# Kernel tuning notes

Measured on AMD Instinct MI355X. Metric: run time of the kernel, lower is better.

Reference implementation:

```python
import jax, jax.numpy as jnp
import numpy as np

B, S, IN, H, NH = 64, 512, 512, 1024, 4
HD = H // NH
A, HID = 18, 1024
EPS = 1e-5


def _ln(x, w, eps=EPS):
    mu = jnp.mean(x, axis=-1, keepdims=True)
    var = jnp.mean((x - mu) ** 2, axis=-1, keepdims=True)
    return (x - mu) * jax.lax.rsqrt(var + eps) * w


def setup_inputs() -> dict:
    key = jax.random.key(0)
    ks = jax.random.split(key, 12)
    g = lambda k, shape, s: jax.random.normal(k, shape, jnp.float32) * s
    return {
        "obs": g(ks[0], (B, S, IN), 1.0),
        "slstm_state": jnp.zeros((4, B, H), jnp.float32),  # (y, c, n, m)
        "W_in": g(ks[1], (H, IN), IN ** -0.5),
        "b_in": jnp.zeros((H,), jnp.float32),
        "ln1_w": jnp.ones((H,), jnp.float32),
        "w_gates": g(ks[2], (4, NH, HD, HD), HD ** -0.5),  # i,f,z,o headwise input proj
        "R": g(ks[3], (NH, HD, 4, HD), HD ** -0.5),        # headwise recurrent kernel
        "b_gates": jnp.zeros((4, H), jnp.float32),
        "gn_w": jnp.ones((H,), jnp.float32),               # multi-head group norm weight
        "ln_post_w": jnp.ones((H,), jnp.float32),          # post-blocks norm
        "W_hid": g(ks[4], (HID, H), H ** -0.5), "b_hid": jnp.zeros((HID,), jnp.float32),
        "W_pol": g(ks[5], (HID, HID), HID ** -0.5), "b_pol": jnp.zeros((HID,), jnp.float32),
        "W_val": g(ks[6], (HID, HID), HID ** -0.5), "b_val": jnp.zeros((HID,), jnp.float32),
        "W_act": g(ks[7], (A, HID), 0.01), "b_act": jnp.zeros((A,), jnp.float32),
        "W_v": g(ks[8], (1, HID), HID ** -0.5), "b_v": jnp.zeros((1,), jnp.float32),
    }


def reference(obs, slstm_state, W_in, b_in, ln1_w, w_gates, R, b_gates, gn_w,
              ln_post_w, W_hid, b_hid, W_pol, b_pol, W_val, b_val, W_act, b_act, W_v, b_v):
    b, s, _ = obs.shape
    # input projection (input_size != hidden_size -> nn.Linear)
    x_proj = obs @ W_in.T + b_in                      # (B,S,H)
    # sLSTM block pre-norm
    xn = _ln(x_proj, ln1_w)
    xh = xn.reshape(b, s, NH, HD)
    # headwise (block-diagonal) gate input preactivations, time-major for scan
    gx = jnp.einsum('bsnd,gnde->sgbne', xh, w_gates)  # (S,4,B,NH,HD)
    bg = b_gates.reshape(4, 1, NH, HD)
    st = slstm_state.reshape(4, b, NH, HD)

    def step(carry, gx_t):
        h, c, n, m = carry
        raw = gx_t + jnp.einsum('bnd,ndge->gbne', h, R) + bg  # (4,B,NH,HD)
        iraw, fraw, zraw, oraw = raw
        logfplusm = m + jax.nn.log_sigmoid(fraw)
        mnew = jnp.maximum(iraw, logfplusm)
        i = jnp.exp(iraw - mnew)
        f = jnp.exp(logfplusm - mnew)
        cnew = f * c + i * jnp.tanh(zraw)
        nnew = f * n + i
        hnew = jax.nn.sigmoid(oraw) * cnew / nnew
        return (hnew, cnew, nnew, mnew), hnew

    _, ys = jax.lax.scan(step, (st[0], st[1], st[2], st[3]), gx)  # (S,B,NH,HD)
    y = jnp.transpose(ys, (1, 0, 2, 3))               # (B,S,NH,HD)
    # multi-head group norm over head_dim, then residual
    mu = jnp.mean(y, axis=-1, keepdims=True)
    var = jnp.mean((y - mu) ** 2, axis=-1, keepdims=True)
    y_gn = (y - mu) * jax.lax.rsqrt(var + EPS) * gn_w.reshape(NH, HD)
    out = x_proj + y_gn.reshape(b, s, H)
    out = _ln(out, ln_post_w)                         # post_blocks_norm
    # actor-critic heads
    hh = jax.nn.relu(out @ W_hid.T + b_hid)
    hp = jax.nn.relu(hh @ W_pol.T + b_pol)
    hv = jax.nn.relu(hh @ W_val.T + b_val)
    logits = hp @ W_act.T + b_act                     # (B,S,A)
    value = hv @ W_v.T + b_v                          # (B,S,1)
    return logits, value
```

## Files before the change

kernel.cpp:

```cpp
#include <hip/hip_runtime.h>
#include <cstdint>
#include <cstddef>

#define B_ 64
#define S_ 512
#define IN_ 512
#define H_ 1024
#define NH_ 4
#define HD_ 256
#define A_ 18
#define HID_ 1024
#define TCH_ 128
#define NCH_ (S_ / TCH_)

using short8 = __attribute__((ext_vector_type(8))) short;
using f32x4  = __attribute__((ext_vector_type(4))) float;

__device__ __forceinline__ unsigned short f2bf(float f) {
  union { float f; unsigned u; } c; c.f = f;
  unsigned r = c.u + 0x7FFFu + ((c.u >> 16) & 1u);
  return (unsigned short)(r >> 16);
}
__device__ __forceinline__ float bf2f(unsigned short h) {
  union { unsigned u; float f; } c; c.u = ((unsigned)h) << 16;
  return c.f;
}
__device__ __forceinline__ unsigned pk2(float a, float b) {
  return (unsigned)f2bf(a) | ((unsigned)f2bf(b) << 16);
}
__device__ __forceinline__ float dot2(unsigned a, unsigned b, float c) {
  float d;
  asm("v_dot2_f32_bf16 %0, %1, %2, %3" : "=v"(d) : "v"(a), "v"(b), "v"(c));
  return d;
}

__global__ __launch_bounds__(256) void rtrans_k(const float* __restrict__ R,
                                                unsigned* __restrict__ Rbb,
                                                unsigned* __restrict__ Rl) {
  const int i = blockIdx.x * 256 + threadIdx.x;
  const int dp = i & 127;
  const int e = (i >> 7) & 255;
  const int g = (i >> 15) & 3;
  const int nh = i >> 17;
  const float* rp = R + (((size_t)nh * 256 + 2 * dp) * 4 + g) * 256 + e;
  unsigned lo = f2bf(rp[0]), hi = f2bf(rp[1024]);
  unsigned v = lo | (hi << 16);
  Rbb[i] = v;
  if (dp >= 96) {
    int j = (dp - 96) >> 1, p = (dp - 96) & 1;
    int col = g * 256 + e;
    Rl[((size_t)(j * 4 + nh) * 1024 + col) * 2 + p] = v;
  }
}

__global__ __launch_bounds__(256) void wgt_k(const float* __restrict__ wg,
                                             unsigned short* __restrict__ wgb) {
  const int i = blockIdx.x * 256 + threadIdx.x;
  const int k = i & 255;
  const int e = (i >> 8) & 255;
  const int g = (i >> 16) & 3;
  const int nh = i >> 18;
  wgb[i] = f2bf(wg[(((size_t)(g * 4 + nh) * 256 + k) * 256) + e]);
}

__global__ __launch_bounds__(256) void wbf_k(const float* __restrict__ src,
                                             unsigned short* __restrict__ dst, int n) {
  int i = blockIdx.x * 256 + threadIdx.x;
  if (i < n) dst[i] = f2bf(src[i]);
}

__global__ __launch_bounds__(256) void rowstats_k(const unsigned short* __restrict__ x,
                                                  float* __restrict__ rs) {
  const int r = blockIdx.x, tid = threadIdx.x;
  const int lane = tid & 63, wave = tid >> 6;
  ushort4 u = *(const ushort4*)(x + (size_t)r * H_ + tid * 4);
  float v0 = bf2f(u.x), v1 = bf2f(u.y), v2 = bf2f(u.z), v3 = bf2f(u.w);
  float s1 = v0 + v1 + v2 + v3;
  float s2 = v0 * v0 + v1 * v1 + v2 * v2 + v3 * v3;
#pragma unroll
  for (int off = 32; off; off >>= 1) { s1 += __shfl_xor(s1, off); s2 += __shfl_xor(s2, off); }
  __shared__ float a1[4], a2[4];
  if (lane == 0) { a1[wave] = s1; a2[wave] = s2; }
  __syncthreads();
  if (tid == 0) {
    float S1 = a1[0] + a1[1] + a1[2] + a1[3];
    float S2 = a2[0] + a2[1] + a2[2] + a2[3];
    float mu = S1 * (1.f / H_);
    float var = S2 * (1.f / H_) - mu * mu;
    rs[r * 2] = mu;
    rs[r * 2 + 1] = rsqrtf(var + 1e-5f);
  }
}

template <int AMODE, int BMODE, bool RELU, int OUTMODE>
__global__ __launch_bounds__(256) void mgemm_k(
    const void* __restrict__ Av, const void* __restrict__ Wv,
    const float* __restrict__ bias, const float* __restrict__ rs,
    const float* __restrict__ lnw, unsigned short* __restrict__ Cb,
    int K, int lda, int chunk) {
  __shared__ uint4 As4[4][128];
  __shared__ uint4 Bs4[4][128];
  const int tid = threadIdx.x;
  const int lane = tid & 63, wave = tid >> 6;
  const int wr = wave >> 1, wc = wave & 1;
  const int col0 = blockIdx.y * 128;
  int nh = 0, g = 0, aoff = 0, bb = 0;
  size_t wbase = 0;
  if constexpr (OUTMODE == 1) {
    int z = blockIdx.z; nh = z >> 2; g = z & 3;
    aoff = nh * HD_;
    bb = blockIdx.x;
    wbase = (size_t)(nh * 4 + g) * 256 * 256;
  }
  auto arow = [&](int mm) -> int {
    if constexpr (OUTMODE == 1) return bb * 512 + chunk * TCH_ + mm;
    else return (int)blockIdx.x * 128 + mm;
  };
  f32x4 acc[4][4];
#pragma unroll
  for (int m = 0; m < 4; ++m)
#pragma unroll
    for (int n = 0; n < 4; ++n) acc[m][n] = 0.f;

  const int sm = tid >> 1;
  const int sh = tid & 1;

  for (int k0 = 0; k0 < K; k0 += 32) {
    {
      int rg = arow(sm);
      unsigned pk[8];
      if constexpr (AMODE == 0) {
        const float* ap = (const float*)Av + (size_t)rg * lda + k0 + sh * 16;
#pragma unroll
        for (int q = 0; q < 4; ++q) {
          float4 f = ((const float4*)ap)[q];
          pk[2 * q] = pk2(f.x, f.y); pk[2 * q + 1] = pk2(f.z, f.w);
        }
      } else if constexpr (AMODE == 1) {
        const uint4* ap = (const uint4*)((const unsigned short*)Av + (size_t)rg * lda + aoff + k0 + sh * 16);
        uint4 u0 = ap[0], u1 = ap[1];
        pk[0] = u0.x; pk[1] = u0.y; pk[2] = u0.z; pk[3] = u0.w;
        pk[4] = u1.x; pk[5] = u1.y; pk[6] = u1.z; pk[7] = u1.w;
      } else {
        const uint4* ap = (const uint4*)((const unsigned short*)Av + (size_t)rg * lda + aoff + k0 + sh * 16);
        uint4 u0 = ap[0], u1 = ap[1];
        unsigned w8[8] = {u0.x, u0.y, u0.z, u0.w, u1.x, u1.y, u1.z, u1.w};
        float mu = rs[rg * 2], rstd = rs[rg * 2 + 1];
        const float* lw = lnw + aoff + k0 + sh * 16;
#pragma unroll
        for (int q = 0; q < 8; ++q) {
          float lo = (bf2f((unsigned short)w8[q]) - mu) * rstd * lw[2 * q];
          float hi = (bf2f((unsigned short)(w8[q] >> 16)) - mu) * rstd * lw[2 * q + 1];
          pk[q] = pk2(lo, hi);
        }
      }
      As4[2 * sh][sm]     = uint4{pk[0], pk[1], pk[2], pk[3]};
      As4[2 * sh + 1][sm] = uint4{pk[4], pk[5], pk[6], pk[7]};
    }
    {
      unsigned pk[8];
      if constexpr (BMODE == 0) {
        const float* wp = (const float*)Wv + (size_t)(col0 + sm) * K + k0 + sh * 16;
#pragma unroll
        for (int q = 0; q < 4; ++q) {
          float4 f = ((const float4*)wp)[q];
          pk[2 * q] = pk2(f.x, f.y); pk[2 * q + 1] = pk2(f.z, f.w);
        }
      } else if constexpr (BMODE == 1) {
        const uint4* wp = (const uint4*)((const unsigned short*)Wv + wbase + (size_t)(col0 + sm) * 256 + k0 + sh * 16);
        uint4 u0 = wp[0], u1 = wp[1];
        pk[0] = u0.x; pk[1] = u0.y; pk[2] = u0.z; pk[3] = u0.w;
        pk[4] = u1.x; pk[5] = u1.y; pk[6] = u1.z; pk[7] = u1.w;
      } else {
        const uint4* wp = (const uint4*)((const unsigned short*)Wv + (size_t)(col0 + sm) * K + k0 + sh * 16);
        uint4 u0 = wp[0], u1 = wp[1];
        pk[0] = u0.x; pk[1] = u0.y; pk[2] = u0.z; pk[3] = u0.w;
        pk[4] = u1.x; pk[5] = u1.y; pk[6] = u1.z; pk[7] = u1.w;
      }
      Bs4[2 * sh][sm]     = uint4{pk[0], pk[1], pk[2], pk[3]};
      Bs4[2 * sh + 1][sm] = uint4{pk[4], pk[5], pk[6], pk[7]};
    }
    __syncthreads();
    short8 af[4], bfv[4];
#pragma unroll
    for (int m = 0; m < 4; ++m)
      af[m] = *(const short8*)&As4[lane >> 4][wr * 64 + m * 16 + (lane & 15)];
#pragma unroll
    for (int n = 0; n < 4; ++n)
      bfv[n] = *(const short8*)&Bs4[lane >> 4][wc * 64 + n * 16 + (lane & 15)];
#pragma unroll
    for (int m = 0; m < 4; ++m)
#pragma unroll
      for (int n = 0; n < 4; ++n)
        acc[m][n] = __builtin_amdgcn_mfma_f32_16x16x32_bf16(af[m], bfv[n], acc[m][n], 0, 0, 0);
    __syncthreads();
  }
  if constexpr (OUTMODE == 0) {
#pragma unroll
    for (int n = 0; n < 4; ++n) {
      int c = col0 + wc * 64 + n * 16 + (lane & 15);
      float bc = bias ? bias[c] : 0.f;
#pragma unroll
      for (int m = 0; m < 4; ++m) {
        int r0 = arow(wr * 64 + m * 16 + ((lane >> 4) << 2));
#pragma unroll
        for (int i = 0; i < 4; ++i) {
          float v = acc[m][n][i] + bc;
          if constexpr (RELU) v = fmaxf(v, 0.f);
          Cb[(size_t)(r0 + i) * 1024 + c] = f2bf(v);
        }
      }
    }
  } else {
#pragma unroll
    for (int n = 0; n < 4; ++n) {
      int e = col0 + wc * 64 + n * 16 + (lane & 15);
#pragma unroll
      for (int m = 0; m < 4; ++m) {
        int sl0 = wr * 64 + m * 16 + ((lane >> 4) << 2);
#pragma unroll
        for (int i = 0; i < 4; ++i) {
          int sl = sl0 + i;
          size_t base = (size_t)(sl * 64 + bb) * 4096 + nh * 1024 + g * 256;
          Cb[base + e] = f2bf(acc[m][n][i]);
        }
      }
    }
  }
}

__global__ __launch_bounds__(1024, 1) void scan_k(
    const unsigned short* __restrict__ gxc, const unsigned* __restrict__ Rbb,
    const unsigned* __restrict__ Rl, const float* __restrict__ bgates,
    float* __restrict__ state, unsigned short* __restrict__ y, int chunk) {
  const int tid = threadIdx.x;
  const int bid = blockIdx.x;
  const int nh = bid >> 6, b = bid & 63;
  const int g = tid >> 8;
  __shared__ uint2 Rlds[16][1024];
  __shared__ float rawf[1024];
  __shared__ alignas(16) unsigned short hsu[256];

#pragma unroll
  for (int j = 0; j < 16; ++j) {
    const uint2* src = (const uint2*)Rl + (size_t)(j * 4 + nh) * 1024 + tid;
    Rlds[j][tid] = *src;
  }
  unsigned rcol[96];
  {
    const unsigned* rp = Rbb + ((size_t)nh * 1024 + tid) * 128;
#pragma unroll
    for (int i = 0; i < 96; ++i) rcol[i] = rp[i];
  }
  const float bg = bgates[g * H_ + nh * HD_ + (tid & 255)];

  const size_t sbase = (size_t)b * H_ + nh * HD_ + tid;
  float c_ = 0.f, n_ = 0.f, m_ = 0.f, hlast = 0.f;
  if (tid < 256) {
    hlast = state[sbase];
    c_ = state[65536 + sbase];
    n_ = state[2 * 65536 + sbase];
    m_ = state[3 * 65536 + sbase];
    hsu[tid] = f2bf(hlast);
  }
  __syncthreads();

  const unsigned short* gp = gxc + ((size_t)b * 4 + nh) * 1024 + tid;
  unsigned short* yp = y + ((size_t)(chunk * TCH_) * 64 + b) * H_ + nh * HD_;

  unsigned short gcur = gp[0];

  for (int t = 0; t < TCH_; ++t) {
    float acc = bf2f(gcur) + bg;
    if (t < TCH_ - 1) gcur = gp[(size_t)(t + 1) * 262144];
    const uint4* h4 = (const uint4*)hsu;
#pragma unroll
    for (int q = 0; q < 24; ++q) {
      uint4 hu = h4[q];
      acc = dot2(rcol[4 * q + 0], hu.x, acc);
      acc = dot2(rcol[4 * q + 1], hu.y, acc);
      acc = dot2(rcol[4 * q + 2], hu.z, acc);
      acc = dot2(rcol[4 * q + 3], hu.w, acc);
    }
#pragma unroll
    for (int s = 0; s < 8; ++s) {
      uint4 hu = h4[24 + s];
      uint2 r0 = Rlds[2 * s][tid];
      uint2 r1 = Rlds[2 * s + 1][tid];
      acc = dot2(r0.x, hu.x, acc);
      acc = dot2(r0.y, hu.y, acc);
      acc = dot2(r1.x, hu.z, acc);
      acc = dot2(r1.y, hu.w, acc);
    }
    float val;
    if (g == 0) {
      val = acc;
    } else if (g == 1) {
      float ls = -log1pf(expf(-fabsf(acc)));
      if (acc < 0.f) ls += acc;
      val = ls;
    } else if (g == 2) {
      val = tanhf(acc);
    } else {
      val = 1.f / (1.f + expf(-acc));
    }
    rawf[tid] = val;
    __syncthreads();
    if (tid < 256) {
      float iraw = rawf[tid];
      float ls   = rawf[256 + tid];
      float tz   = rawf[512 + tid];
      float sg   = rawf[768 + tid];
      float lfm = m_ + ls;
      float mnew = fmaxf(iraw, lfm);
      float iv = expf(iraw - mnew);
      float fv = expf(lfm - mnew);
      c_ = fv * c_ + iv * tz;
      n_ = fv * n_ + iv;
      m_ = mnew;
      hlast = sg * c_ / n_;
      unsigned short hb = f2bf(hlast);
      hsu[tid] = hb;
      yp[(size_t)t * 65536 + tid] = hb;
    }
    __syncthreads();
  }
  if (tid < 256) {
    state[sbase] = hlast;
    state[65536 + sbase] = c_;
    state[2 * 65536 + sbase] = n_;
    state[3 * 65536 + sbase] = m_;
  }
}

__global__ __launch_bounds__(256) void post_k(
    const unsigned short* __restrict__ y, const unsigned short* __restrict__ xp,
    const float* __restrict__ gnw, const float* __restrict__ lpw,
    unsigned short* __restrict__ outb) {
  const int r = blockIdx.x;
  const int b = r >> 9, s = r & 511;
  const int tid = threadIdx.x;
  const int lane = tid & 63, wave = tid >> 6;
  ushort4 yu = *(const ushort4*)(y + (size_t)(s * 64 + b) * H_ + tid * 4);
  float v[4] = {bf2f(yu.x), bf2f(yu.y), bf2f(yu.z), bf2f(yu.w)};
  float s1 = v[0] + v[1] + v[2] + v[3];
  float s2 = v[0] * v[0] + v[1] * v[1] + v[2] * v[2] + v[3] * v[3];
#pragma unroll
  for (int off = 32; off; off >>= 1) { s1 += __shfl_xor(s1, off); s2 += __shfl_xor(s2, off); }
  float mu = s1 * (1.f / HD_);
  float rstd = rsqrtf(s2 * (1.f / HD_) - mu * mu + 1e-5f);
  float4 g4 = *(const float4*)(gnw + tid * 4);
  ushort4 xu = *(const ushort4*)(xp + (size_t)r * H_ + tid * 4);
  float o[4];
  o[0] = fmaf((v[0] - mu) * rstd, g4.x, bf2f(xu.x));
  o[1] = fmaf((v[1] - mu) * rstd, g4.y, bf2f(xu.y));
  o[2] = fmaf((v[2] - mu) * rstd, g4.z, bf2f(xu.z));
  o[3] = fmaf((v[3] - mu) * rstd, g4.w, bf2f(xu.w));
  float t1 = o[0] + o[1] + o[2] + o[3];
  float t2 = o[0] * o[0] + o[1] * o[1] + o[2] * o[2] + o[3] * o[3];
#pragma unroll
  for (int off = 32; off; off >>= 1) { t1 += __shfl_xor(t1, off); t2 += __shfl_xor(t2, off); }
  __shared__ float a1[4], a2[4];
  if (lane == 0) { a1[wave] = t1; a2[wave] = t2; }
  __syncthreads();
  float T1 = a1[0] + a1[1] + a1[2] + a1[3];
  float T2 = a2[0] + a2[1] + a2[2] + a2[3];
  float MU = T1 * (1.f / H_);
  float RS = rsqrtf(T2 * (1.f / H_) - MU * MU + 1e-5f);
  float4 w4 = *(const float4*)(lpw + tid * 4);
  ushort4 res = {f2bf((o[0] - MU) * RS * w4.x), f2bf((o[1] - MU) * RS * w4.y),
                 f2bf((o[2] - MU) * RS * w4.z), f2bf((o[3] - MU) * RS * w4.w)};
  *(ushort4*)(outb + (size_t)r * H_ + tid * 4) = res;
}

__global__ __launch_bounds__(256) void heads_k(
    const unsigned short* __restrict__ hp, const unsigned short* __restrict__ hv,
    const float* __restrict__ Wact, const float* __restrict__ bact,
    const float* __restrict__ Wv, const float* __restrict__ bv,
    float* __restrict__ dout) {
  const int lane = threadIdx.x & 63, wave = threadIdx.x >> 6;
  const int r = blockIdx.x * 4 + wave;
  const unsigned short* hpr = hp + (size_t)r * HID_;
  const unsigned short* hvr = hv + (size_t)r * HID_;
  float acc[A_];
#pragma unroll
  for (int j = 0; j < A_; ++j) acc[j] = 0.f;
  float accv = 0.f;
  for (int i = 0; i < 16; ++i) {
    int k = i * 64 + lane;
    float hpv = bf2f(hpr[k]);
    float hvv = bf2f(hvr[k]);
#pragma unroll
    for (int j = 0; j < A_; ++j) acc[j] = fmaf(hpv, Wact[j * HID_ + k], acc[j]);
    accv = fmaf(hvv, Wv[k], accv);
  }
#pragma unroll
  for (int j = 0; j < A_; ++j)
#pragma unroll
    for (int off = 32; off; off >>= 1) acc[j] += __shfl_xor(acc[j], off);
#pragma unroll
  for (int off = 32; off; off >>= 1) accv += __shfl_xor(accv, off);
  if (lane == 0) {
#pragma unroll
    for (int j = 0; j < A_; ++j) dout[(size_t)r * A_ + j] = acc[j] + bact[j];
    dout[589824 + r] = accv + bv[0];
  }
}

extern "C" void kernel_launch(void* const* d_in, const int* in_sizes, int n_in,
                              void* d_out, int out_size, void* d_ws, size_t ws_size,
                              hipStream_t stream) {
  const float* obs   = (const float*)d_in[0];
  const float* st    = (const float*)d_in[1];
  const float* W_in  = (const float*)d_in[2];
  const float* b_in  = (const float*)d_in[3];
  const float* ln1w  = (const float*)d_in[4];
  const float* wg    = (const float*)d_in[5];
  const float* R     = (const float*)d_in[6];
  const float* bgat  = (const float*)d_in[7];
  const float* gnw   = (const float*)d_in[8];
  const float* lpw   = (const float*)d_in[9];
  const float* W_hid = (const float*)d_in[10];
  const float* b_hid = (const float*)d_in[11];
  const float* W_pol = (const float*)d_in[12];
  const float* b_pol = (const float*)d_in[13];
  const float* W_val = (const float*)d_in[14];
  const float* b_val = (const float*)d_in[15];
  const float* W_act = (const float*)d_in[16];
  const float* b_act = (const float*)d_in[17];
  const float* W_v   = (const float*)d_in[18];
  const float* b_v   = (const float*)d_in[19];

  const size_t NEEDED = 214958080;
  if (ws_size < NEEDED) return;
  char* ws = (char*)d_ws;
  unsigned short* xproj = (unsigned short*)(ws + 0);
  unsigned short* gxc   = (unsigned short*)(ws + 67108864);
  unsigned short* ybuf  = (unsigned short*)(ws + 134217728);
  float* statebuf       = (float*)(ws + 201326592);
  float* rstat          = (float*)(ws + 202375168);
  unsigned* Rbb         = (unsigned*)(ws + 202899456);
  unsigned short* wgb   = (unsigned short*)(ws + 204996608);
  unsigned* Rl          = (unsigned*)(ws + 207093760);
  unsigned short* wib   = (unsigned short*)(ws + 207618048);
  unsigned short* whb   = (unsigned short*)(ws + 208666624);
  unsigned short* wpb   = (unsigned short*)(ws + 210763776);
  unsigned short* wvb   = (unsigned short*)(ws + 212860928);
  unsigned short* outb  = gxc;
  unsigned short* hh    = xproj;
  unsigned short* hp    = ybuf;
  unsigned short* hv    = gxc;
  float* dout = (float*)d_out;

  hipMemcpyAsync(statebuf, st, 4 * 65536 * sizeof(float), hipMemcpyDeviceToDevice, stream);
  rtrans_k<<<2048, 256, 0, stream>>>(R, Rbb, Rl);
  wgt_k<<<4096, 256, 0, stream>>>(wg, wgb);
  wbf_k<<<2048, 256, 0, stream>>>(W_in, wib, 524288);
  wbf_k<<<4096, 256, 0, stream>>>(W_hid, whb, 1048576);
  wbf_k<<<4096, 256, 0, stream>>>(W_pol, wpb, 1048576);
  wbf_k<<<4096, 256, 0, stream>>>(W_val, wvb, 1048576);
  mgemm_k<0, 2, false, 0><<<dim3(256, 8), 256, 0, stream>>>(
      obs, wib, b_in, nullptr, nullptr, xproj, 512, 512, 0);
  rowstats_k<<<32768, 256, 0, stream>>>(xproj, rstat);
  for (int c = 0; c < NCH_; ++c) {
    mgemm_k<2, 1, false, 1><<<dim3(64, 2, 16), 256, 0, stream>>>(
        xproj, wgb, nullptr, rstat, ln1w, gxc, 256, 1024, c);
    scan_k<<<256, 1024, 0, stream>>>(gxc, Rbb, Rl, bgat, statebuf, ybuf, c);
  }
  post_k<<<32768, 256, 0, stream>>>(ybuf, xproj, gnw, lpw, outb);
  mgemm_k<1, 2, true, 0><<<dim3(256, 8), 256, 0, stream>>>(
      outb, whb, b_hid, nullptr, nullptr, hh, 1024, 1024, 0);
  mgemm_k<1, 2, true, 0><<<dim3(256, 8), 256, 0, stream>>>(
      hh, wpb, b_pol, nullptr, nullptr, hp, 1024, 1024, 0);
  mgemm_k<1, 2, true, 0><<<dim3(256, 8), 256, 0, stream>>>(
      hh, wvb, b_val, nullptr, nullptr, hv, 1024, 1024, 0);
  heads_k<<<8192, 256, 0, stream>>>(hp, hv, W_act, b_act, W_v, b_v, dout);
}
```

Before: 2.178 ms.

## Halve scan block size so each thread computes two gate columns

The recurrent scan kernel now runs with 512 threads per block instead of 1024, and each thread owns two of the 1024 gate columns. Each thread holds two register-resident slices of R, shares each h-vector LDS load across both dot products, and runs two independent accumulation chains. Because of the column split, the per-gate activation branches collapse to two fixed cases per thread. The goal is more instruction-level parallelism and fewer waves per block barrier. The cost is roughly double the register pressure (192 R registers plus accumulators), which risks spills, and launch bounds of 512,2 may not be achievable given the LDS footprint.

```diff
diff --git a/kernel.cpp b/kernel.cpp
--- a/kernel.cpp
+++ b/kernel.cpp
@@ -229,30 +229,36 @@
   }
 }
 
-__global__ __launch_bounds__(1024, 1) void scan_k(
+__global__ __launch_bounds__(512, 2) void scan_k(
     const unsigned short* __restrict__ gxc, const unsigned* __restrict__ Rbb,
     const unsigned* __restrict__ Rl, const float* __restrict__ bgates,
     float* __restrict__ state, unsigned short* __restrict__ y, int chunk) {
   const int tid = threadIdx.x;
   const int bid = blockIdx.x;
   const int nh = bid >> 6, b = bid & 63;
-  const int g = tid >> 8;
+  const int col0 = tid, col1 = tid + 512;
+  const int g0 = col0 >> 8, g1 = col1 >> 8;
   __shared__ uint2 Rlds[16][1024];
   __shared__ float rawf[1024];
   __shared__ alignas(16) unsigned short hsu[256];
 
 #pragma unroll
-  for (int j = 0; j < 16; ++j) {
-    const uint2* src = (const uint2*)Rl + (size_t)(j * 4 + nh) * 1024 + tid;
-    Rlds[j][tid] = *src;
-  }
-  unsigned rcol[96];
+  for (int it = 0; it < 32; ++it) {
+    int idx = it * 512 + tid;
+    int j = idx >> 10, col = idx & 1023;
+    Rlds[j][col] = ((const uint2*)Rl)[(size_t)(j * 4 + nh) * 1024 + col];
+  }
+  unsigned rc0[96], rc1[96];
   {
-    const unsigned* rp = Rbb + ((size_t)nh * 1024 + tid) * 128;
-#pragma unroll
-    for (int i = 0; i < 96; ++i) rcol[i] = rp[i];
-  }
-  const float bg = bgates[g * H_ + nh * HD_ + (tid & 255)];
+    const unsigned* rp0 = Rbb + ((size_t)nh * 1024 + col0) * 128;
+    const unsigned* rp1 = Rbb + ((size_t)nh * 1024 + col1) * 128;
+#pragma unroll
+    for (int i = 0; i < 96; ++i) rc0[i] = rp0[i];
+#pragma unroll
+    for (int i = 0; i < 96; ++i) rc1[i] = rp1[i];
+  }
+  const float bg0 = bgates[g0 * H_ + nh * HD_ + (col0 & 255)];
+  const float bg1 = bgates[g1 * H_ + nh * HD_ + (col1 & 255)];
 
   const size_t sbase = (size_t)b * H_ + nh * HD_ + tid;
   float c_ = 0.f, n_ = 0.f, m_ = 0.f, hlast = 0.f;
@@ -265,46 +271,63 @@
   }
   __syncthreads();
 
-  const unsigned short* gp = gxc + ((size_t)b * 4 + nh) * 1024 + tid;
+  const unsigned short* gp0 = gxc + ((size_t)b * 4 + nh) * 1024 + col0;
+  const unsigned short* gp1 = gp0 + 512;
   unsigned short* yp = y + ((size_t)(chunk * TCH_) * 64 + b) * H_ + nh * HD_;
 
-  unsigned short gcur = gp[0];
+  unsigned short gc0 = gp0[0], gc1 = gp1[0];
 
   for (int t = 0; t < TCH_; ++t) {
-    float acc = bf2f(gcur) + bg;
-    if (t < TCH_ - 1) gcur = gp[(size_t)(t + 1) * 262144];
+    float acc0 = bf2f(gc0) + bg0;
+    float acc1 = bf2f(gc1) + bg1;
+    if (t < TCH_ - 1) {
+      gc0 = gp0[(size_t)(t + 1) * 262144];
+      gc1 = gp1[(size_t)(t + 1) * 262144];
+    }
     const uint4* h4 = (const uint4*)hsu;
 #pragma unroll
     for (int q = 0; q < 24; ++q) {
       uint4 hu = h4[q];
-      acc = dot2(rcol[4 * q + 0], hu.x, acc);
-      acc = dot2(rcol[4 * q + 1], hu.y, acc);
-      acc = dot2(rcol[4 * q + 2], hu.z, acc);
-      acc = dot2(rcol[4 * q + 3], hu.w, acc);
+      acc0 = dot2(rc0[4 * q + 0], hu.x, acc0);
+      acc1 = dot2(rc1[4 * q + 0], hu.x, acc1);
+      acc0 = dot2(rc0[4 * q + 1], hu.y, acc0);
+      acc1 = dot2(rc1[4 * q + 1], hu.y, acc1);
+      acc0 = dot2(rc0[4 * q + 2], hu.z, acc0);
+      acc1 = dot2(rc1[4 * q + 2], hu.z, acc1);
+      acc0 = dot2(rc0[4 * q + 3], hu.w, acc0);
+      acc1 = dot2(rc1[4 * q + 3], hu.w, acc1);
     }
 #pragma unroll
     for (int s = 0; s < 8; ++s) {
       uint4 hu = h4[24 + s];
-      uint2 r0 = Rlds[2 * s][tid];
-      uint2 r1 = Rlds[2 * s + 1][tid];
-      acc = dot2(r0.x, hu.x, acc);
-      acc = dot2(r0.y, hu.y, acc);
-      acc = dot2(r1.x, hu.z, acc);
-      acc = dot2(r1.y, hu.w, acc);
-    }
-    float val;
-    if (g == 0) {
-      val = acc;
-    } else if (g == 1) {
-      float ls = -log1pf(expf(-fabsf(acc)));
-      if (acc < 0.f) ls += acc;
-      val = ls;
-    } else if (g == 2) {
-      val = tanhf(acc);
+      uint2 a0 = Rlds[2 * s][col0];
+      uint2 a1 = Rlds[2 * s + 1][col0];
+      uint2 b0 = Rlds[2 * s][col1];
+      uint2 b1 = Rlds[2 * s + 1][col1];
+      acc0 = dot2(a0.x, hu.x, acc0);
+      acc1 = dot2(b0.x, hu.x, acc1);
+      acc0 = dot2(a0.y, hu.y, acc0);
+      acc1 = dot2(b0.y, hu.y, acc1);
+      acc0 = dot2(a1.x, hu.z, acc0);
+      acc1 = dot2(b1.x, hu.z, acc1);
+      acc0 = dot2(a1.y, hu.w, acc0);
+      acc1 = dot2(b1.y, hu.w, acc1);
+    }
+    float val0, val1;
+    if (g0 == 0) {
+      val0 = acc0;
     } else {
-      val = 1.f / (1.f + expf(-acc));
-    }
-    rawf[tid] = val;
+      float ls = -log1pf(expf(-fabsf(acc0)));
+      if (acc0 < 0.f) ls += acc0;
+      val0 = ls;
+    }
+    if (g1 == 2) {
+      val1 = tanhf(acc1);
+    } else {
+      val1 = 1.f / (1.f + expf(-acc1));
+    }
+    rawf[col0] = val0;
+    rawf[col1] = val1;
     __syncthreads();
     if (tid < 256) {
       float iraw = rawf[tid];
@@ -465,7 +488,7 @@
   for (int c = 0; c < NCH_; ++c) {
     mgemm_k<2, 1, false, 1><<<dim3(64, 2, 16), 256, 0, stream>>>(
         xproj, wgb, nullptr, rstat, ln1w, gxc, 256, 1024, c);
-    scan_k<<<256, 1024, 0, stream>>>(gxc, Rbb, Rl, bgat, statebuf, ybuf, c);
+    scan_k<<<256, 512, 0, stream>>>(gxc, Rbb, Rl, bgat, statebuf, ybuf, c);
   }
   post_k<<<32768, 256, 0, stream>>>(ybuf, xproj, gnw, lpw, outb);
   mgemm_k<1, 2, true, 0><<<dim3(256, 8), 256, 0, stream>>>(
```

Result: faster. 2.067 ms (-5.1%).
